# Kernel tuning notes

Measured on AMD Instinct MI355X. Metric: run time of the kernel, lower is better.

Reference implementation:

```python
import jax, jax.numpy as jnp
import numpy as np

V, E, HID, D = 10000, 512, 512, 14
FEAT = 512  # attention feature dim (== C)


def setup_inputs() -> dict:
    key = jax.random.key(0)
    ks = jax.random.split(key, 20)
    s = 0.02
    inp = {
        "features": jax.random.normal(ks[0], (32, 512, 7, 7), jnp.float32),
        "captions": jax.random.randint(ks[1], (32, 60), 0, V),
        "disease": jax.random.uniform(ks[2], (32, D), jnp.float32),
        # embedding
        "emb": jax.random.normal(ks[3], (V, E), jnp.float32) * s,
        # attention: attn Linear(feat+hid -> hid), v Linear(hid -> 1)
        "W_attn": jax.random.normal(ks[4], (FEAT + HID, HID), jnp.float32) * s,
        "b_attn": jnp.zeros((HID,), jnp.float32),
        "W_v": jax.random.normal(ks[5], (HID, 1), jnp.float32) * s,
        "b_v": jnp.zeros((1,), jnp.float32),
        # attention disease_proj: 14->128->512
        "W_dp1": jax.random.normal(ks[6], (D, 128), jnp.float32) * s,
        "b_dp1": jnp.zeros((128,), jnp.float32),
        "W_dp2": jax.random.normal(ks[7], (128, HID), jnp.float32) * s,
        "b_dp2": jnp.zeros((HID,), jnp.float32),
        # disease_encoder: 14->128->256 (dropout = identity at eval)
        "W_de1": jax.random.normal(ks[8], (D, 128), jnp.float32) * s,
        "b_de1": jnp.zeros((128,), jnp.float32),
        "W_de2": jax.random.normal(ks[9], (128, 256), jnp.float32) * s,
        "b_de2": jnp.zeros((256,), jnp.float32),
        # LSTM (input = E + 512 + 256 = 1280), gate order i,f,g,o
        "W_ih": jax.random.normal(ks[10], (E + FEAT + 256, 4 * HID), jnp.float32) * s,
        "W_hh": jax.random.normal(ks[11], (HID, 4 * HID), jnp.float32) * s,
        "b_ih": jnp.zeros((4 * HID,), jnp.float32),
        "b_hh": jnp.zeros((4 * HID,), jnp.float32),
        # fc: hid -> vocab
        "W_fc": jax.random.normal(ks[12], (HID, V), jnp.float32) * s,
        "b_fc": jnp.zeros((V,), jnp.float32),
    }
    return inp


def reference(features, captions, disease, emb, W_attn, b_attn, W_v, b_v,
              W_dp1, b_dp1, W_dp2, b_dp2, W_de1, b_de1, W_de2, b_de2,
              W_ih, W_hh, b_ih, b_hh, W_fc, b_fc):
    B, C = features.shape[0], features.shape[1]
    f = features.reshape(B, C, -1).transpose(0, 2, 1)  # [B, N, 512]

    embs = emb[captions]  # [B, T, E]

    # time-invariant disease contexts
    dis_ctx = jax.nn.relu(disease @ W_de1 + b_de1) @ W_de2 + b_de2   # [B,256]
    dis_att = jax.nn.relu(disease @ W_dp1 + b_dp1) @ W_dp2 + b_dp2  # [B,HID]

    # split attn weight: energy = tanh(f@Wf + (h+dis_att)@Wh + b)
    Wf, Wh = W_attn[:FEAT], W_attn[FEAT:]
    f_proj = jnp.einsum('bnf,fh->bnh', f, Wf)  # precompute feature part

    def step(carry, emb_t):
        h, c = carry  # [B,HID] each
        hid = h + dis_att
        energy = jnp.tanh(f_proj + (hid @ Wh + b_attn)[:, None, :])  # [B,N,HID]
        scores = (energy @ W_v).squeeze(-1) + b_v[0]                 # [B,N]
        alpha = jax.nn.softmax(scores, axis=1)
        context = jnp.einsum('bn,bnf->bf', alpha, f)                 # [B,512]
        x = jnp.concatenate([emb_t, context, dis_ctx], axis=1)       # [B,1280]
        gates = x @ W_ih + h @ W_hh + b_ih + b_hh
        i, fg, g, o = jnp.split(gates, 4, axis=1)
        c_new = jax.nn.sigmoid(fg) * c + jax.nn.sigmoid(i) * jnp.tanh(g)
        h_new = jax.nn.sigmoid(o) * jnp.tanh(c_new)
        return (h_new, c_new), h_new

    h0 = jnp.zeros((B, HID), f.dtype)
    c0 = jnp.zeros((B, HID), f.dtype)
    _, h_seq = jax.lax.scan(step, (h0, c0), embs.transpose(1, 0, 2))  # [T,B,HID]

    logits = h_seq @ W_fc + b_fc          # [T,B,V]
    return logits.transpose(1, 0, 2)      # [B,T,V]
```

## Files before the change

### kernel.cpp

```cpp
#include <hip/hip_runtime.h>
#include <math.h>

#define BB 32
#define NP 49
#define FE 512
#define HI 512
#define EM 512
#define TT 60
#define G4 2048
#define NV 10000
#define ND 14
#define NBLK 80

typedef __attribute__((ext_vector_type(8))) short short8v;
typedef __attribute__((ext_vector_type(4))) float float4v;

__device__ __forceinline__ float fsig(float x){ return 1.0f/(1.0f+__expf(-x)); }
__device__ __forceinline__ float ftanh(float x){
    x = fminf(fmaxf(x, -15.0f), 15.0f);
    float e = __expf(2.0f*x);
    return (e-1.0f)/(e+1.0f);
}
__device__ __forceinline__ ushort f2bf(float x){
    union { float f; unsigned u; } v; v.f = x;
    unsigned r = v.u + 0x7fff + ((v.u >> 16) & 1);
    return (ushort)(r >> 16);
}
__device__ __forceinline__ float bf2f(ushort h){
    union { float f; unsigned u; } v; v.u = ((unsigned)h) << 16;
    return v.f;
}
__device__ __forceinline__ ushort f2bf_trunc(float x){
    return (ushort)(__float_as_uint(x) >> 16);
}

__global__ void k_transpose(const float* __restrict__ feat, float* __restrict__ fT){
    int b = blockIdx.y;
    int cb = blockIdx.x * 64;
    __shared__ float tile[64][NP+1];
    const float* src = feat + (size_t)b*FE*NP;
    for (int idx = threadIdx.x; idx < 64*NP; idx += 256){
        int cl = idx / NP, n = idx % NP;
        tile[cl][n] = src[(size_t)(cb+cl)*NP + n];
    }
    __syncthreads();
    float* dst = fT + (size_t)b*NP*FE;
    for (int idx = threadIdx.x; idx < 64*NP; idx += 256){
        int cl = idx % 64, n = idx / 64;
        dst[(size_t)n*FE + cb + cl] = tile[cl][n];
    }
}

__global__ void k_disease(const float* __restrict__ dis,
                          const float* __restrict__ Wdp1, const float* __restrict__ bdp1,
                          const float* __restrict__ Wdp2, const float* __restrict__ bdp2,
                          const float* __restrict__ Wde1, const float* __restrict__ bde1,
                          const float* __restrict__ Wde2, const float* __restrict__ bde2,
                          const float* __restrict__ Wattn, const float* __restrict__ battn,
                          const float* __restrict__ Wih, const float* __restrict__ bih,
                          const float* __restrict__ bhh,
                          float* __restrict__ daw, float* __restrict__ disWih){
    int b = blockIdx.x;
    int tid = threadIdx.x;
    __shared__ float d[ND];
    __shared__ float hp[128], he[128];
    __shared__ float datt[HI];
    __shared__ float dctx[256];
    if (tid < ND) d[tid] = dis[b*ND + tid];
    __syncthreads();
    if (tid < 128){
        float accP = bdp1[tid], accE = bde1[tid];
        for (int k=0;k<ND;k++){ accP += d[k]*Wdp1[k*128+tid]; accE += d[k]*Wde1[k*128+tid]; }
        hp[tid] = fmaxf(accP, 0.f);
        he[tid] = fmaxf(accE, 0.f);
    }
    __syncthreads();
    for (int j = tid; j < HI; j += 256){
        float a = bdp2[j];
        for (int k=0;k<128;k++) a += hp[k]*Wdp2[k*HI+j];
        datt[j] = a;
    }
    if (tid < 256){
        float a = bde2[tid];
        for (int k=0;k<128;k++) a += he[k]*Wde2[k*256+tid];
        dctx[tid] = a;
    }
    __syncthreads();
    for (int j = tid; j < HI; j += 256){
        float a = battn[j];
        for (int k=0;k<HI;k++) a += datt[k]*Wattn[(size_t)(FE+k)*HI + j];
        daw[b*HI + j] = a;
    }
    for (int j = tid; j < G4; j += 256){
        float a = bih[j] + bhh[j];
        for (int k=0;k<256;k++) a += dctx[k]*Wih[(size_t)(EM+FE+k)*G4 + j];
        disWih[b*G4 + j] = a;
    }
}

__global__ void k_fproj(const float* __restrict__ fT, const float* __restrict__ Wattn,
                        float* __restrict__ f_proj){
    int b = blockIdx.y, ng = blockIdx.x;
    int n0 = ng*7;
    __shared__ float fr[7][FE];
    const float* src = fT + ((size_t)b*NP + n0)*FE;
    for (int idx = threadIdx.x; idx < 7*FE; idx += 256)
        fr[idx/FE][idx%FE] = src[idx];
    __syncthreads();
    int j0 = threadIdx.x;
    float acc[7][2];
    #pragma unroll
    for (int n=0;n<7;n++){ acc[n][0]=0.f; acc[n][1]=0.f; }
    for (int k=0;k<FE;k++){
        float w0 = Wattn[(size_t)k*HI + j0];
        float w1 = Wattn[(size_t)k*HI + j0 + 256];
        #pragma unroll
        for (int n=0;n<7;n++){
            float fv = fr[n][k];
            acc[n][0] += fv*w0;
            acc[n][1] += fv*w1;
        }
    }
    float* dst = f_proj + ((size_t)b*NP + n0)*HI;
    #pragma unroll
    for (int n=0;n<7;n++){
        dst[(size_t)n*HI + j0] = acc[n][0];
        dst[(size_t)n*HI + j0+256] = acc[n][1];
    }
}

__global__ void k_fwc(const float* __restrict__ fT, const float* __restrict__ Wih,
                      float* __restrict__ fWcP){
    int b = blockIdx.z, ng = blockIdx.y, half = blockIdx.x;
    int n0 = ng*7;
    __shared__ float fr[7][FE];
    const float* src = fT + ((size_t)b*NP + n0)*FE;
    for (int idx = threadIdx.x; idx < 7*FE; idx += 256)
        fr[idx/FE][idx%FE] = src[idx];
    __syncthreads();
    int j0 = half*1024 + threadIdx.x;
    float acc[7][4];
    #pragma unroll
    for (int n=0;n<7;n++){ acc[n][0]=0.f; acc[n][1]=0.f; acc[n][2]=0.f; acc[n][3]=0.f; }
    const float* W = Wih + (size_t)512*G4;
    for (int k=0;k<FE;k++){
        float w0=W[(size_t)k*G4+j0], w1=W[(size_t)k*G4+j0+256], w2=W[(size_t)k*G4+j0+512], w3=W[(size_t)k*G4+j0+768];
        #pragma unroll
        for (int n=0;n<7;n++){
            float fv = fr[n][k];
            acc[n][0]+=fv*w0; acc[n][1]+=fv*w1; acc[n][2]+=fv*w2; acc[n][3]+=fv*w3;
        }
    }
    for (int n=0;n<7;n++){
        #pragma unroll
        for (int q=0;q<4;q++){
            int gc = j0 + q*256;
            int blk = (gc & 511) >> 3, m = gc & 7, g = gc >> 9;
            fWcP[(((size_t)blk*BB + b)*NP + n0+n)*32 + m*4+g] = acc[n][q];
        }
    }
}

__global__ void k_preg(const int* __restrict__ caps, const float* __restrict__ emb,
                       const float* __restrict__ Wih, const float* __restrict__ disWih,
                       float* __restrict__ preGP){
    int rg = blockIdx.y;
    int jt = blockIdx.x;
    int r0 = rg*16;
    __shared__ float er[16][EM];
    __shared__ int bidx[16];
    if (threadIdx.x < 16) bidx[threadIdx.x] = caps[r0 + threadIdx.x];
    __syncthreads();
    for (int idx = threadIdx.x; idx < 16*EM; idx += 256){
        int rl = idx >> 9, k = idx & 511;
        er[rl][k] = emb[(size_t)bidx[rl]*EM + k];
    }
    __syncthreads();
    int j = jt*512 + threadIdx.x;
    float acc[16][2];
    #pragma unroll
    for (int r=0;r<16;r++){ acc[r][0]=0.f; acc[r][1]=0.f; }
    for (int k=0;k<EM;k+=2){
        float w00 = Wih[(size_t)k*G4 + j],     w10 = Wih[(size_t)k*G4 + j + 256];
        float w01 = Wih[(size_t)(k+1)*G4 + j], w11 = Wih[(size_t)(k+1)*G4 + j + 256];
        #pragma unroll
        for (int r=0;r<16;r++){
            float2 e = *(const float2*)&er[r][k];
            acc[r][0] += e.x*w00 + e.y*w01;
            acc[r][1] += e.x*w10 + e.y*w11;
        }
    }
    for (int r=0;r<16;r++){
        int row = r0 + r;
        int b = row/60, t = row - b*60;
        #pragma unroll
        for (int q=0;q<2;q++){
            int gc = j + q*256;
            float v = acc[r][q] + disWih[b*G4 + gc];
            int blk = (gc & 511) >> 3, m = gc & 7, g = gc >> 9;
            preGP[(((size_t)blk*TT + t)*BB + b)*32 + m*4+g] = v;
        }
    }
}

__device__ __forceinline__ void gridbar(int* bar, int tgt){
    __syncthreads();
    if (threadIdx.x == 0){
        __threadfence();
        __hip_atomic_store(bar + blockIdx.x, tgt, __ATOMIC_RELAXED, __HIP_MEMORY_SCOPE_AGENT);
    }
    if (blockIdx.x == 0 && threadIdx.x < 64){
        int l = threadIdx.x;
        for (;;){
            int v0 = __hip_atomic_load(bar + l, __ATOMIC_RELAXED, __HIP_MEMORY_SCOPE_AGENT);
            int v1 = (l < NBLK-64) ? __hip_atomic_load(bar + 64 + l, __ATOMIC_RELAXED, __HIP_MEMORY_SCOPE_AGENT) : tgt;
            if (__all(v0 >= tgt && v1 >= tgt)) break;
            __builtin_amdgcn_s_sleep(1);
        }
        if (l == 0)
            __hip_atomic_store(bar + 128, tgt, __ATOMIC_RELAXED, __HIP_MEMORY_SCOPE_AGENT);
    }
    if (threadIdx.x == 0){
        while (__hip_atomic_load(bar + 128, __ATOMIC_RELAXED, __HIP_MEMORY_SCOPE_AGENT) < tgt)
            __builtin_amdgcn_s_sleep(1);
        __threadfence();
    }
    __syncthreads();
}

__launch_bounds__(512, 1)
__global__ void k_scan_coop(const float* __restrict__ f_proj, const float* __restrict__ fWcP,
                            const float* __restrict__ preGP, const float* __restrict__ daw,
                            const float* __restrict__ Wattn, const float* __restrict__ Whh,
                            const float* __restrict__ Wv,
                            float* __restrict__ h_seq, float* __restrict__ a_buf,
                            float* __restrict__ scores, int* __restrict__ bar){
    __shared__ __align__(16) ushort h_hi[16384], h_lo[16384];
    __shared__ __align__(16) ushort w_hi[16384], w_lo[16384];
    __shared__ float al[32*52];
    __shared__ float gbuf[32*33];
    __shared__ float daw_lds[32*32];
    __shared__ float gv[32*36];
    __shared__ float cst[256];
    __shared__ float wvl[512];
    int bk = blockIdx.x;
    int tid = threadIdx.x;
    int lane = tid & 63, wave = tid >> 6;
    bool isGate = bk < 64;

    {
        int k = tid;
        if (isGate){
            const float* wr = Whh + (size_t)k*G4 + bk*8;
            #pragma unroll
            for (int g = 0; g < 4; g++){
                float4 v0 = *(const float4*)(wr + g*512);
                float4 v1 = *(const float4*)(wr + g*512 + 4);
                float vv[8] = {v0.x,v0.y,v0.z,v0.w,v1.x,v1.y,v1.z,v1.w};
                #pragma unroll
                for (int u = 0; u < 8; u++){
                    int c = u*4 + g;
                    ushort hi = f2bf(vv[u]);
                    ushort lo = f2bf(vv[u] - bf2f(hi));
                    int idx = (c*512 + k) ^ ((c&7)<<3);
                    w_hi[idx] = hi; w_lo[idx] = lo;
                }
            }
        } else {
            const float* wr = Wattn + (size_t)(FE + k)*HI + (bk-64)*32;
            #pragma unroll
            for (int cq = 0; cq < 8; cq++){
                float4 v = *(const float4*)(wr + cq*4);
                float vv[4] = {v.x,v.y,v.z,v.w};
                #pragma unroll
                for (int q = 0; q < 4; q++){
                    int c = cq*4 + q;
                    ushort hi = f2bf(vv[q]);
                    ushort lo = f2bf(vv[q] - bf2f(hi));
                    int idx = (c*512 + k) ^ ((c&7)<<3);
                    w_hi[idx] = hi; w_lo[idx] = lo;
                }
            }
            for (int i = tid; i < 1024; i += 512){
                int b = i >> 5, c = i & 31;
                daw_lds[i] = daw[b*HI + (bk-64)*32 + c];
            }
        }
        if (tid < 256) cst[tid] = 0.f;
        wvl[tid] = Wv[tid];
    }
    __syncthreads();

    int tgt = 0;
    for (int t = 0; t < TT; t++){
        if (t == 0){
            uint4 z = make_uint4(0,0,0,0);
            #pragma unroll
            for (int it = 0; it < 4; it++){
                int flat = (it*512 + tid)*8;
                int b = flat >> 9, k = flat & 511;
                int di = (b*512 + k) ^ ((b&7)<<3);
                *(uint4*)&h_hi[di] = z;
                *(uint4*)&h_lo[di] = z;
            }
        } else {
            const float* hs = h_seq + (size_t)(t-1)*BB*HI;
            #pragma unroll
            for (int it = 0; it < 4; it++){
                int flat = (it*512 + tid)*8;
                int b = flat >> 9, k = flat & 511;
                float4 v0 = *(const float4*)(hs + flat);
                float4 v1 = *(const float4*)(hs + flat + 4);
                float fv[8] = {v0.x,v0.y,v0.z,v0.w,v1.x,v1.y,v1.z,v1.w};
                union { ushort u[8]; uint4 v; } ph, pl;
                #pragma unroll
                for (int j = 0; j < 8; j++){
                    ushort hi = f2bf(fv[j]);
                    ph.u[j] = hi;
                    pl.u[j] = f2bf(fv[j] - bf2f(hi));
                }
                int di = (b*512 + k) ^ ((b&7)<<3);
                *(uint4*)&h_hi[di] = ph.v;
                *(uint4*)&h_lo[di] = pl.v;
            }
        }
        __syncthreads();

        if (wave < 4){
            int rbase = (wave >> 1) * 16, cbase = (wave & 1) * 16;
            int m = lane & 15, kg = lane >> 4;
            int arow = rbase + m, bcol = cbase + m;
            int abase = arow*512 + kg*8, axr = (arow&7)<<3;
            int bbase = bcol*512 + kg*8, bxr = (bcol&7)<<3;
            float4v acc = {0.f,0.f,0.f,0.f};
            #pragma unroll
            for (int ks = 0; ks < 16; ks++){
                int ai = (abase + ks*32) ^ axr;
                int bi = (bbase + ks*32) ^ bxr;
                short8v ahi = *(const short8v*)&h_hi[ai];
                short8v alo = *(const short8v*)&h_lo[ai];
                short8v bhi = *(const short8v*)&w_hi[bi];
                short8v blo = *(const short8v*)&w_lo[bi];
                acc = __builtin_amdgcn_mfma_f32_16x16x32_bf16(ahi, bhi, acc, 0,0,0);
                acc = __builtin_amdgcn_mfma_f32_16x16x32_bf16(alo, bhi, acc, 0,0,0);
                acc = __builtin_amdgcn_mfma_f32_16x16x32_bf16(ahi, blo, acc, 0,0,0);
            }
            int ccol = cbase + (lane & 15);
            int crow0 = rbase + (lane >> 4)*4;
            if (isGate){
                #pragma unroll
                for (int r = 0; r < 4; r++)
                    gbuf[(crow0+r)*33 + ccol] = acc[r];
            } else {
                int cb = (bk-64)*32;
                float* ab = a_buf + (size_t)t*BB*HI;
                #pragma unroll
                for (int r = 0; r < 4; r++)
                    ab[(size_t)(crow0+r)*HI + cb + ccol] = acc[r] + daw_lds[(crow0+r)*32 + ccol];
            }
        }
        gridbar(bar, ++tgt);

        {
            int wid = tid >> 6, l = tid & 63;
            for (int p = bk + wid*NBLK; p < BB*NP; p += NBLK*8){
                int pb = p / NP, pn = p - pb*NP;
                const float* fpn = f_proj + ((size_t)pb*NP + pn)*HI;
                const float* at  = a_buf + ((size_t)t*BB + pb)*HI;
                int j = l*8;
                float4 f0 = *(const float4*)(fpn + j);
                float4 a0 = *(const float4*)(at + j);
                float4 f1 = *(const float4*)(fpn + j + 4);
                float4 a1 = *(const float4*)(at + j + 4);
                float s = wvl[j+0]*ftanh(f0.x + a0.x)
                        + wvl[j+1]*ftanh(f0.y + a0.y)
                        + wvl[j+2]*ftanh(f0.z + a0.z)
                        + wvl[j+3]*ftanh(f0.w + a0.w)
                        + wvl[j+4]*ftanh(f1.x + a1.x)
                        + wvl[j+5]*ftanh(f1.y + a1.y)
                        + wvl[j+6]*ftanh(f1.z + a1.z)
                        + wvl[j+7]*ftanh(f1.w + a1.w);
                #pragma unroll
                for (int off = 32; off; off >>= 1) s += __shfl_xor(s, off);
                if (l == 0) scores[t*(BB*NP) + p] = s;
            }
        }
        gridbar(bar, ++tgt);

        if (isGate){
            int hw = tid >> 5, l32 = tid & 31;
            #pragma unroll
            for (int rep = 0; rep < 2; rep++){
                int b = hw + rep*16;
                const float* sb = scores + t*(BB*NP) + b*NP;
                float s0 = sb[l32];
                float s1 = (l32 < 17) ? sb[32 + l32] : -1e30f;
                float m = fmaxf(s0, s1);
                #pragma unroll
                for (int off = 16; off; off >>= 1) m = fmaxf(m, __shfl_xor(m, off, 32));
                float e0 = __expf(s0 - m);
                float e1 = (l32 < 17) ? __expf(s1 - m) : 0.f;
                float sm = e0 + e1;
                #pragma unroll
                for (int off = 16; off; off >>= 1) sm += __shfl_xor(sm, off, 32);
                float inv = 1.f / sm;
                al[b*52 + l32] = e0*inv;
                if (l32 < 17) al[b*52 + 32 + l32] = e1*inv;
            }
            __syncthreads();
            {
                int b = tid >> 4, cp = tid & 15;
                float g0 = gbuf[b*33 + cp];
                float g1 = gbuf[b*33 + cp + 16];
                const float* pgp = preGP + (((size_t)bk*TT + t)*BB + b)*32;
                g0 += pgp[cp];
                g1 += pgp[cp + 16];
                const float* fw = fWcP + (((size_t)bk*BB + b)*NP)*32;
                for (int n = 0; n < NP; n++){
                    float av = al[b*52 + n];
                    g0 += av*fw[n*32 + cp];
                    g1 += av*fw[n*32 + cp + 16];
                }
                gv[b*36 + cp]      = g0;
                gv[b*36 + cp + 16] = g1;
            }
            __syncthreads();
            if (tid < 256){
                int b = tid >> 3, m = tid & 7;
                float gi = gv[b*36 + m*4 + 0];
                float gf = gv[b*36 + m*4 + 1];
                float gg = gv[b*36 + m*4 + 2];
                float go = gv[b*36 + m*4 + 3];
                float cn = fsig(gf)*cst[b*8 + m] + fsig(gi)*ftanh(gg);
                float hn = fsig(go)*ftanh(cn);
                cst[b*8 + m] = cn;
                h_seq[(size_t)t*BB*HI + b*HI + bk*8 + m] = hn;
            }
        }
        gridbar(bar, ++tgt);
    }
}

__launch_bounds__(512, 1)
__global__ void k_logits(const float* __restrict__ h_seq, const float* __restrict__ Wfc,
                         const float* __restrict__ bfc, float* __restrict__ out){
    __shared__ __align__(16) ushort h_hi[16384], h_lo[16384];
    int t = blockIdx.x, vt = blockIdx.y;
    int tid = threadIdx.x, lane = tid & 63, wave = tid >> 6;
    const float* hs = h_seq + (size_t)t*BB*HI;
    #pragma unroll
    for (int it = 0; it < 4; it++){
        int flat = (it*512 + tid)*8;
        int b = flat >> 9, k = flat & 511;
        float4 v0 = *(const float4*)(hs + flat);
        float4 v1 = *(const float4*)(hs + flat + 4);
        float fv[8] = {v0.x,v0.y,v0.z,v0.w,v1.x,v1.y,v1.z,v1.w};
        union { ushort u[8]; uint4 v; } ph, pl;
        #pragma unroll
        for (int j = 0; j < 8; j++){
            ushort hi = f2bf(fv[j]);
            ph.u[j] = hi;
            pl.u[j] = f2bf(fv[j] - bf2f(hi));
        }
        int di = (b*512 + k) ^ ((b&7)<<3);
        *(uint4*)&h_hi[di] = ph.v;
        *(uint4*)&h_lo[di] = pl.v;
    }
    __syncthreads();

    int m = lane & 15, kg = lane >> 4;
    int cb = vt*256 + wave*32;
    int a0 = m*512 + kg*8;
    int a1 = (16+m)*512 + kg*8;
    int axr = (m&7)<<3;
    float4v acc[2][2];
    acc[0][0]=(float4v){0,0,0,0}; acc[0][1]=(float4v){0,0,0,0};
    acc[1][0]=(float4v){0,0,0,0}; acc[1][1]=(float4v){0,0,0,0};
    const short8v bz = {0,0,0,0,0,0,0,0};

    for (int ks = 0; ks < 16; ks++){
        short8v ah0 = *(const short8v*)&h_hi[(a0 + ks*32) ^ axr];
        short8v al0 = *(const short8v*)&h_lo[(a0 + ks*32) ^ axr];
        short8v ah1 = *(const short8v*)&h_hi[(a1 + ks*32) ^ axr];
        short8v al1 = *(const short8v*)&h_lo[(a1 + ks*32) ^ axr];
        #pragma unroll
        for (int cj = 0; cj < 2; cj++){
            int v = cb + cj*16 + m;
            short8v bhi = bz, blo = bz;
            if (v < NV){
                int k0 = ks*32 + kg*8;
                const float* wp = Wfc + (size_t)k0*NV + v;
                float w[8];
                #pragma unroll
                for (int i = 0; i < 8; i++) w[i] = wp[(size_t)i*NV];
                union { ushort u[8]; short8v s; } bh, bl;
                #pragma unroll
                for (int i = 0; i < 8; i++){
                    ushort hi = f2bf(w[i]);
                    bh.u[i] = hi;
                    bl.u[i] = f2bf_trunc(w[i] - bf2f(hi));
                }
                bhi = bh.s; blo = bl.s;
            }
            acc[0][cj] = __builtin_amdgcn_mfma_f32_16x16x32_bf16(ah0, bhi, acc[0][cj], 0,0,0);
            acc[0][cj] = __builtin_amdgcn_mfma_f32_16x16x32_bf16(al0, bhi, acc[0][cj], 0,0,0);
            acc[0][cj] = __builtin_amdgcn_mfma_f32_16x16x32_bf16(ah0, blo, acc[0][cj], 0,0,0);
            acc[1][cj] = __builtin_amdgcn_mfma_f32_16x16x32_bf16(ah1, bhi, acc[1][cj], 0,0,0);
            acc[1][cj] = __builtin_amdgcn_mfma_f32_16x16x32_bf16(al1, bhi, acc[1][cj], 0,0,0);
            acc[1][cj] = __builtin_amdgcn_mfma_f32_16x16x32_bf16(ah1, blo, acc[1][cj], 0,0,0);
        }
    }
    #pragma unroll
    for (int cj = 0; cj < 2; cj++){
        int v = cb + cj*16 + m;
        if (v < NV){
            float bias = bfc[v];
            #pragma unroll
            for (int ri = 0; ri < 2; ri++){
                int b0 = ri*16 + kg*4;
                #pragma unroll
                for (int r = 0; r < 4; r++)
                    out[((size_t)(b0+r)*TT + t)*NV + v] = acc[ri][cj][r] + bias;
            }
        }
    }
}

extern "C" void kernel_launch(void* const* d_in, const int* in_sizes, int n_in,
                              void* d_out, int out_size, void* d_ws, size_t ws_size,
                              hipStream_t stream){
    const float* features = (const float*)d_in[0];
    const int*   captions = (const int*)d_in[1];
    const float* disease  = (const float*)d_in[2];
    const float* emb      = (const float*)d_in[3];
    const float* W_attn   = (const float*)d_in[4];
    const float* b_attn   = (const float*)d_in[5];
    const float* W_v      = (const float*)d_in[6];
    const float* W_dp1    = (const float*)d_in[8];
    const float* b_dp1    = (const float*)d_in[9];
    const float* W_dp2    = (const float*)d_in[10];
    const float* b_dp2    = (const float*)d_in[11];
    const float* W_de1    = (const float*)d_in[12];
    const float* b_de1    = (const float*)d_in[13];
    const float* W_de2    = (const float*)d_in[14];
    const float* b_de2    = (const float*)d_in[15];
    const float* W_ih     = (const float*)d_in[16];
    const float* W_hh     = (const float*)d_in[17];
    const float* b_ih     = (const float*)d_in[18];
    const float* b_hh     = (const float*)d_in[19];
    const float* W_fc     = (const float*)d_in[20];
    const float* b_fc     = (const float*)d_in[21];
    float* out = (float*)d_out;

    const size_t N_HSEQ = (size_t)TT*BB*HI;
    float* h_seq = (float*)d_ws;
    int*   bar   = (int*)((char*)d_ws + N_HSEQ*sizeof(float));

    const size_t N_FT   = (size_t)BB*NP*FE;
    const size_t N_FP   = (size_t)BB*NP*HI;
    const size_t N_FWC  = (size_t)BB*NP*G4;
    const size_t N_PREG = (size_t)BB*TT*G4;
    const size_t N_ABUF = (size_t)TT*BB*HI;
    const size_t N_SC   = (size_t)TT*BB*NP;
    float* fT     = out;
    float* f_proj = fT + N_FT;
    float* fWcP   = f_proj + N_FP;
    float* preGP  = fWcP + N_FWC;
    float* a_buf  = preGP + N_PREG;
    float* scores = a_buf + N_ABUF;
    float* disWih = scores + N_SC;
    float* daw    = disWih + (size_t)BB*G4;

    hipMemsetAsync(bar, 0, 1024, stream);
    k_transpose<<<dim3(8,BB),256,0,stream>>>(features, fT);
    k_disease<<<BB,256,0,stream>>>(disease, W_dp1,b_dp1,W_dp2,b_dp2,
                                   W_de1,b_de1,W_de2,b_de2,
                                   W_attn,b_attn, W_ih,b_ih,b_hh,
                                   daw, disWih);
    k_fproj<<<dim3(7,BB),256,0,stream>>>(fT, W_attn, f_proj);
    k_fwc<<<dim3(2,7,BB),256,0,stream>>>(fT, W_ih, fWcP);
    k_preg<<<dim3(4,120),256,0,stream>>>(captions, emb, W_ih, disWih, preGP);
    k_scan_coop<<<NBLK,512,0,stream>>>(f_proj, fWcP, preGP, daw,
                                       W_attn, W_hh, W_v,
                                       h_seq, a_buf, scores, bar);
    k_logits<<<dim3(TT,40),512,0,stream>>>(h_seq, W_fc, b_fc, out);
}
```

Baseline: 1.987 ms.

## Fuse attention score partials into attention blocks, removing one grid barrier per step

The 16 attention blocks now compute partial attention scores over their own 32-column slice of the hidden projection, using a column-blocked f_proj layout. Each block writes per-slice partials that the gate blocks sum after the next barrier. Previously every block round-tripped the full a_buf and then computed the scores. This cuts one grid-wide barrier per timestep and the a_buf global traffic. In exchange it adds a 16-way partial-sum reduction in the gate blocks and concentrates the tanh work on the 16 attention blocks.

```diff
diff --git a/kernel.cpp b/kernel.cpp
--- a/kernel.cpp
+++ b/kernel.cpp
@@ -11,6 +11,7 @@
 #define NV 10000
 #define ND 14
 #define NBLK 80
+#define NPAIR (BB*NP)
 
 typedef __attribute__((ext_vector_type(8))) short short8v;
 typedef __attribute__((ext_vector_type(4))) float float4v;
@@ -99,7 +100,7 @@
 }
 
 __global__ void k_fproj(const float* __restrict__ fT, const float* __restrict__ Wattn,
-                        float* __restrict__ f_proj){
+                        float* __restrict__ f_projB){
     int b = blockIdx.y, ng = blockIdx.x;
     int n0 = ng*7;
     __shared__ float fr[7][FE];
@@ -121,11 +122,12 @@
             acc[n][1] += fv*w1;
         }
     }
-    float* dst = f_proj + ((size_t)b*NP + n0)*HI;
+    int j1 = j0 + 256;
     #pragma unroll
     for (int n=0;n<7;n++){
-        dst[(size_t)n*HI + j0] = acc[n][0];
-        dst[(size_t)n*HI + j0+256] = acc[n][1];
+        int p = b*NP + n0 + n;
+        f_projB[((size_t)(j0>>5)*NPAIR + p)*32 + (j0&31)] = acc[n][0];
+        f_projB[((size_t)(j1>>5)*NPAIR + p)*32 + (j1&31)] = acc[n][1];
     }
 }
 
@@ -229,24 +231,25 @@
 }
 
 __launch_bounds__(512, 1)
-__global__ void k_scan_coop(const float* __restrict__ f_proj, const float* __restrict__ fWcP,
+__global__ void k_scan_coop(const float* __restrict__ f_projB, const float* __restrict__ fWcP,
                             const float* __restrict__ preGP, const float* __restrict__ daw,
                             const float* __restrict__ Wattn, const float* __restrict__ Whh,
                             const float* __restrict__ Wv,
-                            float* __restrict__ h_seq, float* __restrict__ a_buf,
-                            float* __restrict__ scores, int* __restrict__ bar){
+                            float* __restrict__ h_seq, float* __restrict__ scoresP,
+                            int* __restrict__ bar){
     __shared__ __align__(16) ushort h_hi[16384], h_lo[16384];
     __shared__ __align__(16) ushort w_hi[16384], w_lo[16384];
     __shared__ float al[32*52];
     __shared__ float gbuf[32*33];
-    __shared__ float daw_lds[32*32];
+    __shared__ float uni[NPAIR];
     __shared__ float gv[32*36];
     __shared__ float cst[256];
-    __shared__ float wvl[512];
+    __shared__ float wvl[32];
     int bk = blockIdx.x;
     int tid = threadIdx.x;
     int lane = tid & 63, wave = tid >> 6;
     bool isGate = bk < 64;
+    int bkA = bk - 64;
 
     {
         int k = tid;
@@ -267,7 +270,7 @@
                 }
             }
         } else {
-            const float* wr = Wattn + (size_t)(FE + k)*HI + (bk-64)*32;
+            const float* wr = Wattn + (size_t)(FE + k)*HI + bkA*32;
             #pragma unroll
             for (int cq = 0; cq < 8; cq++){
                 float4 v = *(const float4*)(wr + cq*4);
@@ -283,11 +286,11 @@
             }
             for (int i = tid; i < 1024; i += 512){
                 int b = i >> 5, c = i & 31;
-                daw_lds[i] = daw[b*HI + (bk-64)*32 + c];
-            }
+                uni[i] = daw[b*HI + bkA*32 + c];
+            }
+            if (tid < 32) wvl[tid] = Wv[bkA*32 + tid];
         }
         if (tid < 256) cst[tid] = 0.f;
-        wvl[tid] = Wv[tid];
     }
     __syncthreads();
 
@@ -352,77 +355,90 @@
                 for (int r = 0; r < 4; r++)
                     gbuf[(crow0+r)*33 + ccol] = acc[r];
             } else {
-                int cb = (bk-64)*32;
-                float* ab = a_buf + (size_t)t*BB*HI;
                 #pragma unroll
                 for (int r = 0; r < 4; r++)
-                    ab[(size_t)(crow0+r)*HI + cb + ccol] = acc[r] + daw_lds[(crow0+r)*32 + ccol];
-            }
+                    gbuf[(crow0+r)*33 + ccol] = acc[r] + uni[(crow0+r)*32 + ccol];
+            }
+        }
+        __syncthreads();
+
+        float g0r = 0.f, g1r = 0.f;
+        if (!isGate){
+            const float* fB = f_projB + (size_t)bkA*NPAIR*32;
+            float* spt = scoresP + ((size_t)t*16 + bkA)*NPAIR;
+            #pragma unroll
+            for (int it = 0; it < 4; it++){
+                int p = it*512 + tid;
+                if (p < NPAIR){
+                    int pb = (int)((unsigned)p/49u);
+                    const float* ga = &gbuf[pb*33];
+                    const float4* f4 = (const float4*)(fB + (size_t)p*32);
+                    float s = 0.f;
+                    #pragma unroll
+                    for (int c4 = 0; c4 < 8; c4++){
+                        float4 fv = f4[c4];
+                        int c = c4*4;
+                        s += wvl[c+0]*ftanh(fv.x + ga[c+0])
+                           + wvl[c+1]*ftanh(fv.y + ga[c+1])
+                           + wvl[c+2]*ftanh(fv.z + ga[c+2])
+                           + wvl[c+3]*ftanh(fv.w + ga[c+3]);
+                    }
+                    spt[p] = s;
+                }
+            }
+        } else {
+            int b = tid >> 4, cp = tid & 15;
+            const float* pgp = preGP + (((size_t)bk*TT + t)*BB + b)*32;
+            g0r = gbuf[b*33 + cp] + pgp[cp];
+            g1r = gbuf[b*33 + cp + 16] + pgp[cp + 16];
         }
         gridbar(bar, ++tgt);
 
-        {
-            int wid = tid >> 6, l = tid & 63;
-            for (int p = bk + wid*NBLK; p < BB*NP; p += NBLK*8){
-                int pb = p / NP, pn = p - pb*NP;
-                const float* fpn = f_proj + ((size_t)pb*NP + pn)*HI;
-                const float* at  = a_buf + ((size_t)t*BB + pb)*HI;
-                int j = l*8;
-                float4 f0 = *(const float4*)(fpn + j);
-                float4 a0 = *(const float4*)(at + j);
-                float4 f1 = *(const float4*)(fpn + j + 4);
-                float4 a1 = *(const float4*)(at + j + 4);
-                float s = wvl[j+0]*ftanh(f0.x + a0.x)
-                        + wvl[j+1]*ftanh(f0.y + a0.y)
-                        + wvl[j+2]*ftanh(f0.z + a0.z)
-                        + wvl[j+3]*ftanh(f0.w + a0.w)
-                        + wvl[j+4]*ftanh(f1.x + a1.x)
-                        + wvl[j+5]*ftanh(f1.y + a1.y)
-                        + wvl[j+6]*ftanh(f1.z + a1.z)
-                        + wvl[j+7]*ftanh(f1.w + a1.w);
-                #pragma unroll
-                for (int off = 32; off; off >>= 1) s += __shfl_xor(s, off);
-                if (l == 0) scores[t*(BB*NP) + p] = s;
-            }
-        }
-        gridbar(bar, ++tgt);
-
         if (isGate){
-            int hw = tid >> 5, l32 = tid & 31;
-            #pragma unroll
-            for (int rep = 0; rep < 2; rep++){
-                int b = hw + rep*16;
-                const float* sb = scores + t*(BB*NP) + b*NP;
-                float s0 = sb[l32];
-                float s1 = (l32 < 17) ? sb[32 + l32] : -1e30f;
-                float m = fmaxf(s0, s1);
-                #pragma unroll
-                for (int off = 16; off; off >>= 1) m = fmaxf(m, __shfl_xor(m, off, 32));
-                float e0 = __expf(s0 - m);
-                float e1 = (l32 < 17) ? __expf(s1 - m) : 0.f;
-                float sm = e0 + e1;
-                #pragma unroll
-                for (int off = 16; off; off >>= 1) sm += __shfl_xor(sm, off, 32);
-                float inv = 1.f / sm;
-                al[b*52 + l32] = e0*inv;
-                if (l32 < 17) al[b*52 + 32 + l32] = e1*inv;
+            const float* spt = scoresP + (size_t)t*16*NPAIR;
+            #pragma unroll
+            for (int it = 0; it < 4; it++){
+                int p = it*512 + tid;
+                if (p < NPAIR){
+                    float s = 0.f;
+                    #pragma unroll
+                    for (int k2 = 0; k2 < 16; k2++) s += spt[(size_t)k2*NPAIR + p];
+                    uni[p] = s;
+                }
+            }
+            __syncthreads();
+            {
+                int hw = tid >> 5, l32 = tid & 31;
+                #pragma unroll
+                for (int rep = 0; rep < 2; rep++){
+                    int b = hw + rep*16;
+                    const float* sb = uni + b*NP;
+                    float s0 = sb[l32];
+                    float s1 = (l32 < 17) ? sb[32 + l32] : -1e30f;
+                    float m = fmaxf(s0, s1);
+                    #pragma unroll
+                    for (int off = 16; off; off >>= 1) m = fmaxf(m, __shfl_xor(m, off, 32));
+                    float e0 = __expf(s0 - m);
+                    float e1 = (l32 < 17) ? __expf(s1 - m) : 0.f;
+                    float sm = e0 + e1;
+                    #pragma unroll
+                    for (int off = 16; off; off >>= 1) sm += __shfl_xor(sm, off, 32);
+                    float inv = 1.f / sm;
+                    al[b*52 + l32] = e0*inv;
+                    if (l32 < 17) al[b*52 + 32 + l32] = e1*inv;
+                }
             }
             __syncthreads();
             {
                 int b = tid >> 4, cp = tid & 15;
-                float g0 = gbuf[b*33 + cp];
-                float g1 = gbuf[b*33 + cp + 16];
-                const float* pgp = preGP + (((size_t)bk*TT + t)*BB + b)*32;
-                g0 += pgp[cp];
-                g1 += pgp[cp + 16];
                 const float* fw = fWcP + (((size_t)bk*BB + b)*NP)*32;
                 for (int n = 0; n < NP; n++){
                     float av = al[b*52 + n];
-                    g0 += av*fw[n*32 + cp];
-                    g1 += av*fw[n*32 + cp + 16];
-                }
-                gv[b*36 + cp]      = g0;
-                gv[b*36 + cp + 16] = g1;
+                    g0r += av*fw[n*32 + cp];
+                    g1r += av*fw[n*32 + cp + 16];
+                }
+                gv[b*36 + cp]      = g0r;
+                gv[b*36 + cp + 16] = g1r;
             }
             __syncthreads();
             if (tid < 256){
@@ -557,18 +573,16 @@
     int*   bar   = (int*)((char*)d_ws + N_HSEQ*sizeof(float));
 
     const size_t N_FT   = (size_t)BB*NP*FE;
-    const size_t N_FP   = (size_t)BB*NP*HI;
+    const size_t N_FPB  = (size_t)16*NPAIR*32;
     const size_t N_FWC  = (size_t)BB*NP*G4;
     const size_t N_PREG = (size_t)BB*TT*G4;
-    const size_t N_ABUF = (size_t)TT*BB*HI;
-    const size_t N_SC   = (size_t)TT*BB*NP;
+    const size_t N_SCP  = (size_t)TT*16*NPAIR;
     float* fT     = out;
-    float* f_proj = fT + N_FT;
-    float* fWcP   = f_proj + N_FP;
+    float* f_projB= fT + N_FT;
+    float* fWcP   = f_projB + N_FPB;
     float* preGP  = fWcP + N_FWC;
-    float* a_buf  = preGP + N_PREG;
-    float* scores = a_buf + N_ABUF;
-    float* disWih = scores + N_SC;
+    float* scoresP= preGP + N_PREG;
+    float* disWih = scoresP + N_SCP;
     float* daw    = disWih + (size_t)BB*G4;
 
     hipMemsetAsync(bar, 0, 1024, stream);
@@ -577,11 +591,11 @@
                                    W_de1,b_de1,W_de2,b_de2,
                                    W_attn,b_attn, W_ih,b_ih,b_hh,
                                    daw, disWih);
-    k_fproj<<<dim3(7,BB),256,0,stream>>>(fT, W_attn, f_proj);
+    k_fproj<<<dim3(7,BB),256,0,stream>>>(fT, W_attn, f_projB);
     k_fwc<<<dim3(2,7,BB),256,0,stream>>>(fT, W_ih, fWcP);
     k_preg<<<dim3(4,120),256,0,stream>>>(captions, emb, W_ih, disWih, preGP);
-    k_scan_coop<<<NBLK,512,0,stream>>>(f_proj, fWcP, preGP, daw,
+    k_scan_coop<<<NBLK,512,0,stream>>>(f_projB, fWcP, preGP, daw,
                                        W_attn, W_hh, W_v,
-                                       h_seq, a_buf, scores, bar);
+                                       h_seq, scoresP, bar);
     k_logits<<<dim3(TT,40),512,0,stream>>>(h_seq, W_fc, b_fc, out);
 }
```

New measurement: 2.474 ms. +24.6%, slower.
